# Kernel tuning notes

Hardware: AMD Instinct MI355X
Metric: run time of the kernel (lower is better)

## Reference

```python
import jax, jax.numpy as jnp
import numpy as np

B, DF, H, W = 32, 8, 144, 144
OFF = 2
K = 2 * OFF + 1            # window width 5
DS, DT, NC = 512, 1024, 6
HEADS, DH, MLP = 16, 64, 2048
THR = 0.3
CIN = DF * W               # 1152, Conv1d in-channels
ITC = DF * H * K           # 5760, token feature size
EPS = 1e-5


def _heads(X, w1, b1, g, bt, mu, vr, w2, b2):
    # X: (B, CIN, H). Per-class 1x1 conv -> BatchNorm(eval stats) -> 1x1 conv -> softmax over last dim.
    h = jnp.einsum('bch,ksc->bksh', X, w1) + b1[None, :, :, None]
    h = (h - mu[None, :, :, None]) * (g / jnp.sqrt(vr + EPS))[None, :, :, None] + bt[None, :, :, None]
    lg = jnp.einsum('bksh,kos->bkoh', h, w2) + b2[None, :, :, None]
    return jax.nn.softmax(jnp.swapaxes(lg, 2, 3), axis=-1)   # (B, NC, H, O)


def _ln(z, g, b):
    m = z.mean(-1, keepdims=True)
    v = ((z - m) ** 2).mean(-1, keepdims=True)
    return (z - m) / jnp.sqrt(v + EPS) * g + b


def _forward(x, ext_w1, ext_b1, ext_g, ext_bt, ext_mu, ext_vr, ext_w2, ext_b2, cls_w1, cls_b1, cls_g, cls_bt, cls_mu, cls_vr, cls_w2, cls_b2, ext2_w1, ext2_b1, ext2_g, ext2_bt, ext2_mu, ext2_vr, ext2_w2, ext2_b2, cls2_w1, cls2_b1, cls2_g, cls2_bt, cls2_mu, cls2_vr, cls2_w2, cls2_b2, emb, tok_w, tok_b, ln1_g, ln1_b, qkv_w, out_w, out_b, ln2_g, ln2_b, ff_w1, ff_b1, ff_w2, ff_b2, lnf_g, lnf_b, dec_w, dec_b):
    X = x.transpose(0, 1, 3, 2).reshape(B, CIN, H)          # 'b c h w -> b (c w) h'
    ext = _heads(X, ext_w1, ext_b1, ext_g, ext_bt, ext_mu, ext_vr, ext_w2, ext_b2)   # (B,NC,H,2)
    cls = _heads(X, cls_w1, cls_b1, cls_g, cls_bt, cls_mu, cls_vr, cls_w2, cls_b2)   # (B,NC,H,W)

    exist = jnp.mean(ext[..., 0], axis=2) > THR             # (B,NC) lane-existence threshold
    corr = jnp.argmax(cls, axis=-1)                         # (B,NC,H) per-row column index

    TRASH = W + 2 * OFF                                     # start of discard region for masked writes
    pad = jnp.pad(x, ((0, 0), (0, 0), (0, 0), (OFF, OFF + K)))  # left/right zero pad + K trash cols
    cols = corr[..., None] + jnp.arange(K)                  # (B,NC,H,K) window cols in padded coords
    win = jnp.take_along_axis(pad[:, None], jnp.broadcast_to(cols[:, :, None], (B, NC, DF, H, K)), axis=4)  # (B,NC,DF,H,K)

    tok = win.reshape(B, NC, ITC) @ tok_w.T + tok_b + emb[None]   # (B,NC,DT)

    # transformer depth 1; non-existing lane tokens are masked out as keys (exact match to
    # running attention over only the existing tokens, since there is no positional encoding)
    y = _ln(tok, ln1_g, ln1_b)
    qkv = y @ qkv_w.T
    q, k, v = jnp.split(qkv, 3, axis=-1)
    q = q.reshape(B, NC, HEADS, DH).transpose(0, 2, 1, 3)
    k = k.reshape(B, NC, HEADS, DH).transpose(0, 2, 1, 3)
    v = v.reshape(B, NC, HEADS, DH).transpose(0, 2, 1, 3)
    s = jnp.einsum('bhnd,bhmd->bhnm', q, k) * (DH ** -0.5)
    s = jnp.where(exist[:, None, None, :], s, -1e9)
    a = jax.nn.softmax(s, axis=-1)
    o = jnp.einsum('bhnm,bhmd->bhnd', a, v).transpose(0, 2, 1, 3).reshape(B, NC, HEADS * DH)
    tok = tok + o @ out_w.T + out_b
    y = _ln(tok, ln2_g, ln2_b)
    tok = tok + jax.nn.gelu(y @ ff_w1.T + ff_b1, approximate=False) @ ff_w2.T + ff_b2
    dec = (_ln(tok, lnf_g, lnf_b) @ dec_w.T + dec_b).reshape(B, NC, DF, H, K)

    # sequential per-class windowed write-back; rows limited to H-1 to reproduce the
    # original's `for idx_h in range(idx_h)` loop bound; masked lanes write to trash cols
    hmask = jnp.arange(H) < (H - 1)
    bi = jnp.arange(B)[:, None, None]
    hi = jnp.arange(H)[None, :, None]
    for c in range(NC):
        m = exist[:, c, None] & hmask[None, :]                          # (B,H)
        cc = jnp.where(m[:, :, None], cols[:, c], TRASH + jnp.arange(K))
        pad = pad.at[bi, :, hi, cc].set(dec[:, c].transpose(0, 2, 3, 1))  # vals (B,H,K,DF)
    x2 = pad[:, :, :, OFF:OFF + W]

    X2 = x2.transpose(0, 1, 3, 2).reshape(B, CIN, H)
    ext2 = _heads(X2, ext2_w1, ext2_b1, ext2_g, ext2_bt, ext2_mu, ext2_vr, ext2_w2, ext2_b2)
    cls2 = _heads(X2, cls2_w1, cls2_b1, cls2_g, cls2_bt, cls2_mu, cls2_vr, cls2_w2, cls2_b2)
    return ext, cls, ext2, cls2


def setup_inputs():
    ks = iter(jax.random.split(jax.random.key(0), 64))
    def w(*s):
        return jax.random.normal(next(ks), s, dtype=jnp.float32) * 0.02
    d = {"x": jax.random.normal(next(ks), (B, DF, H, W), dtype=jnp.float32)}
    for p in ["ext", "cls", "ext2", "cls2"]:
        O = 2 if p.startswith("ext") else W
        d[p + "_w1"] = w(NC, DS, CIN); d[p + "_b1"] = jnp.zeros((NC, DS))
        d[p + "_g"] = jnp.ones((NC, DS)); d[p + "_bt"] = jnp.zeros((NC, DS))
        d[p + "_mu"] = jnp.zeros((NC, DS)); d[p + "_vr"] = jnp.ones((NC, DS))
        d[p + "_w2"] = w(NC, O, DS); d[p + "_b2"] = jnp.zeros((NC, O))
    INNER = HEADS * DH
    d["emb"] = w(NC, DT); d["tok_w"] = w(DT, ITC); d["tok_b"] = jnp.zeros((DT,))
    d["ln1_g"] = jnp.ones((DT,)); d["ln1_b"] = jnp.zeros((DT,))
    d["qkv_w"] = w(3 * INNER, DT); d["out_w"] = w(DT, INNER); d["out_b"] = jnp.zeros((DT,))
    d["ln2_g"] = jnp.ones((DT,)); d["ln2_b"] = jnp.zeros((DT,))
    d["ff_w1"] = w(MLP, DT); d["ff_b1"] = jnp.zeros((MLP,))
    d["ff_w2"] = w(DT, MLP); d["ff_b2"] = jnp.zeros((DT,))
    d["lnf_g"] = jnp.ones((DT,)); d["lnf_b"] = jnp.zeros((DT,))
    d["dec_w"] = w(ITC, DT); d["dec_b"] = jnp.zeros((ITC,))
    return d


def reference(x, ext_w1, ext_b1, ext_g, ext_bt, ext_mu, ext_vr, ext_w2, ext_b2, cls_w1, cls_b1, cls_g, cls_bt, cls_mu, cls_vr, cls_w2, cls_b2, ext2_w1, ext2_b1, ext2_g, ext2_bt, ext2_mu, ext2_vr, ext2_w2, ext2_b2, cls2_w1, cls2_b1, cls2_g, cls2_bt, cls2_mu, cls2_vr, cls2_w2, cls2_b2, emb, tok_w, tok_b, ln1_g, ln1_b, qkv_w, out_w, out_b, ln2_g, ln2_b, ff_w1, ff_b1, ff_w2, ff_b2, lnf_g, lnf_b, dec_w, dec_b):
    return _forward(x, ext_w1, ext_b1, ext_g, ext_bt, ext_mu, ext_vr, ext_w2, ext_b2, cls_w1, cls_b1, cls_g, cls_bt, cls_mu, cls_vr, cls_w2, cls_b2, ext2_w1, ext2_b1, ext2_g, ext2_bt, ext2_mu, ext2_vr, ext2_w2, ext2_b2, cls2_w1, cls2_b1, cls2_g, cls2_bt, cls2_mu, cls2_vr, cls2_w2, cls2_b2, emb, tok_w, tok_b, ln1_g, ln1_b, qkv_w, out_w, out_b, ln2_g, ln2_b, ff_w1, ff_b1, ff_w2, ff_b2, lnf_g, lnf_b, dec_w, dec_b)
```

## Files before the change

kernel.cpp:

```cpp
#include <hip/hip_runtime.h>
#include <math.h>

#define Bb 32
#define DFc 8
#define Hh 144
#define Ww 144
#define OFFc 2
#define KWc 5
#define DSc 512
#define DTc 1024
#define NCc 6
#define HEADSc 16
#define DHc 64
#define MLPc 2048
#define CINc (DFc * Ww)
#define ITCc (DFc * Hh * KWc)
#define BHc (Bb * Hh)
#define INNERc (HEADSc * DHc)
#define EPSc 1e-5f
#define THRc 0.3f
#define WLNc 4608
#define GAPDELTA 1e-3f

typedef __attribute__((ext_vector_type(8))) short short8;
typedef __attribute__((ext_vector_type(4))) float f32x4;

#define ATOMIC_ADD_F32(p, v) unsafeAtomicAdd((p), (v))

__device__ inline unsigned short f2bf(float v) {
    unsigned int u = __float_as_uint(v);
    unsigned int r = (u + 0x7FFFu + ((u >> 16) & 1u)) >> 16;
    return (unsigned short)r;
}
__device__ inline float bf2f(unsigned short b) {
    return __uint_as_float(((unsigned int)b) << 16);
}

__global__ void k_split_x(const float* __restrict__ x, unsigned short* __restrict__ p,
                          long planeStride)
{
    int tid = blockIdx.x * 256 + threadIdx.x;
    if (tid >= BHc * CINc) return;
    int n = tid / CINc, k = tid % CINc;
    int b = n / Hh, h = n % Hh;
    int f = k / Ww, w = k % Ww;
    float v = x[((long)(b * DFc + f) * Hh + h) * Ww + w];
    unsigned short h0 = f2bf(v);
    p[tid] = h0;
    p[planeStride + tid] = f2bf(v - bf2f(h0));
}

__global__ __launch_bounds__(256) void k_transpose(
    const float* __restrict__ src, float* __restrict__ dst)
{
    __shared__ float t[32][33];
    const int nc = blockIdx.z;
    const int s0 = blockIdx.y * 32;
    const int k0 = blockIdx.x * 32;
    const int lx = threadIdx.x & 31, ly = threadIdx.x >> 5;
    const float* sp = src + ((long)nc * 512 + s0) * 1152 + k0;
#pragma unroll
    for (int i = 0; i < 32; i += 8)
        t[ly + i][lx] = sp[(long)(ly + i) * 1152 + lx];
    __syncthreads();
    float* dp = dst + ((long)nc * 1152 + k0) * 512 + s0;
#pragma unroll
    for (int i = 0; i < 32; i += 8)
        dp[(long)(ly + i) * 512 + lx] = t[lx][ly + i];
}

__global__ void k_w2s(const float* __restrict__ w2, const float* __restrict__ scale,
                      float* __restrict__ Ws, int O, int Mpad)
{
    int i = blockIdx.x * 256 + threadIdx.x;
    if (i >= NCc * Mpad * 512) return;
    int s = i & 511;
    int o = (i >> 9) % Mpad;
    int nc = i / (Mpad * 512);
    float v = 0.f;
    if (o < O) v = w2[((long)nc * O + o) * 512 + s] * scale[nc * 512 + s];
    Ws[i] = v;
}

__global__ __launch_bounds__(256) void gemm_nt_b(
    const float* __restrict__ A, long sAz,
    const float* __restrict__ Bm, long sBz,
    float* __restrict__ C, long sCz, int K)
{
    __shared__ float As[16][68];
    __shared__ float Bs[16][68];
    const int tid = threadIdx.x;
    const int n0 = blockIdx.x * 64;
    const int m0 = blockIdx.y * 64;
    const int z = blockIdx.z;
    const int lRow = tid >> 2, lCol = (tid & 3) << 2;
    const int ty = tid >> 4, tx = tid & 15;
    const float* Az = A + (long)z * sAz;
    const float* Bz = Bm + (long)z * sBz;

    float acc[4][4];
#pragma unroll
    for (int i = 0; i < 4; i++)
#pragma unroll
        for (int j = 0; j < 4; j++) acc[i][j] = 0.f;

    for (int k0 = 0; k0 < K; k0 += 16) {
        float4 av = *(const float4*)(Az + (long)(m0 + lRow) * K + k0 + lCol);
        As[lCol + 0][lRow] = av.x; As[lCol + 1][lRow] = av.y;
        As[lCol + 2][lRow] = av.z; As[lCol + 3][lRow] = av.w;
        float4 bv = *(const float4*)(Bz + (long)(n0 + lRow) * K + k0 + lCol);
        Bs[lCol + 0][lRow] = bv.x; Bs[lCol + 1][lRow] = bv.y;
        Bs[lCol + 2][lRow] = bv.z; Bs[lCol + 3][lRow] = bv.w;
        __syncthreads();
#pragma unroll
        for (int kk = 0; kk < 16; kk++) {
            float4 a = *(const float4*)&As[kk][ty * 4];
            float4 b = *(const float4*)&Bs[kk][tx * 4];
            float aa[4] = {a.x, a.y, a.z, a.w};
            float bb[4] = {b.x, b.y, b.z, b.w};
#pragma unroll
            for (int i = 0; i < 4; i++)
#pragma unroll
                for (int j = 0; j < 4; j++) acc[i][j] += aa[i] * bb[j];
        }
        __syncthreads();
    }
    const int ncol = n0 + tx * 4;
#pragma unroll
    for (int i = 0; i < 4; i++) {
        float* cp = C + (long)z * sCz + (long)(m0 + ty * 4 + i) * 1152 + ncol;
#pragma unroll
        for (int j = 0; j < 4; j++) cp[j] = acc[i][j];
    }
}

__global__ __launch_bounds__(256) void k_effb(
    const float* __restrict__ w2c, const float* __restrict__ b2c, const float* __restrict__ shiftC,
    const float* __restrict__ w2e, const float* __restrict__ b2e, const float* __restrict__ shiftE,
    float* __restrict__ effB)
{
    int g = blockIdx.x * 16 + (threadIdx.x >> 4);
    int lane = threadIdx.x & 15;
    if (g >= NCc * 256) return;
    int nc = g >> 8, o = g & 255;
    float d = 0.f;
    if (o < 144) {
        const float* wp = w2c + ((long)nc * 144 + o) * 512;
        const float* sp = shiftC + nc * 512;
        for (int s = lane; s < 512; s += 16) d += wp[s] * sp[s];
    } else if (o < 146) {
        const float* wp = w2e + ((long)nc * 2 + (o - 144)) * 512;
        const float* sp = shiftE + nc * 512;
        for (int s = lane; s < 512; s += 16) d += wp[s] * sp[s];
    }
#pragma unroll
    for (int off = 8; off; off >>= 1) d += __shfl_xor(d, off);
    if (lane == 0) {
        float b = (o < 144) ? b2c[nc * 144 + o] : ((o < 146) ? b2e[nc * 2 + o - 144] : 0.f);
        effB[g] = d + b;
    }
}

__global__ void k_split_effw(const float* __restrict__ effW, unsigned short* __restrict__ p,
                             long planeStride)
{
    int i = blockIdx.x * 256 + threadIdx.x;
    if (i >= NCc * 256 * 1152) return;
    int o = (i / 1152) & 255;
    float v = (o < 208) ? effW[i] : 0.f;
    unsigned short h0 = f2bf(v);
    p[i] = h0;
    p[planeStride + i] = f2bf(v - bf2f(h0));
}

__global__ __launch_bounds__(256) void gemm_fused(
    const unsigned short* __restrict__ Ag, long strideA,
    const unsigned short* __restrict__ Bg, long strideB,
    float* __restrict__ lgT, float* __restrict__ extLg,
    const float* __restrict__ effB)
{
    constexpr int K = 1152;
    constexpr int PAt[3] = {0, 0, 1};
    constexpr int PBt[3] = {0, 1, 0};
    __shared__ __align__(16) unsigned short As[2][2][128 * 32];
    __shared__ __align__(16) unsigned short Bs[2][2][128 * 32];
    const int tid = threadIdx.x;
    const int w = tid >> 6;
    const int l = tid & 63;
    const int quad = l >> 4, l15 = l & 15;
    const int z = blockIdx.z;
    const int m0 = blockIdx.y * 128, n0 = blockIdx.x * 128;
    const int rw = (w >> 1) * 64, cw = (w & 1) * 64;

    f32x4 acc[4][4];
#pragma unroll
    for (int i = 0; i < 4; i++)
#pragma unroll
        for (int j = 0; j < 4; j++) acc[i][j] = (f32x4){0.f, 0.f, 0.f, 0.f};

    const int srow = w * 32;
    const int lr = l >> 2;
    const int lc = ((l & 3) ^ ((lr >> 1) & 3)) * 8;
    const unsigned short* gA[2];
    const unsigned short* gB[2];
#pragma unroll
    for (int p = 0; p < 2; p++) {
        gA[p] = Ag + (long)p * strideA + ((long)(z * 256 + m0 + srow + lr)) * K + lc;
        gB[p] = Bg + (long)p * strideB + ((long)(n0 + srow + lr)) * K + lc;
    }
    const int ldsOff0 = srow * 32;
    const int ldsOff1 = (srow + 16) * 32;
    const int rdoff = (quad ^ ((l15 >> 1) & 3)) * 8;

    auto STAGE = [&](int buf, int k0) {
#pragma unroll
        for (int p = 0; p < 2; p++) {
            __builtin_amdgcn_global_load_lds(
                (const __attribute__((address_space(1))) void*)(gA[p] + k0),
                (__attribute__((address_space(3))) void*)&As[buf][p][ldsOff0], 16, 0, 0);
            __builtin_amdgcn_global_load_lds(
                (const __attribute__((address_space(1))) void*)(gA[p] + 16 * K + k0),
                (__attribute__((address_space(3))) void*)&As[buf][p][ldsOff1], 16, 0, 0);
            __builtin_amdgcn_global_load_lds(
                (const __attribute__((address_space(1))) void*)(gB[p] + k0),
                (__attribute__((address_space(3))) void*)&Bs[buf][p][ldsOff0], 16, 0, 0);
            __builtin_amdgcn_global_load_lds(
                (const __attribute__((address_space(1))) void*)(gB[p] + 16 * K + k0),
                (__attribute__((address_space(3))) void*)&Bs[buf][p][ldsOff1], 16, 0, 0);
        }
    };

    const int nk = K >> 5;
    STAGE(0, 0);
    __syncthreads();
    int cur = 0;
    for (int t = 0; t < nk; ++t) {
        if (t + 1 < nk) STAGE(cur ^ 1, (t + 1) << 5);

        short8 af[2][4], bf[2][4];
#pragma unroll
        for (int p = 0; p < 2; p++)
#pragma unroll
            for (int i = 0; i < 4; i++) {
                af[p][i] = *(const short8*)&As[cur][p][(rw + i * 16 + l15) * 32 + rdoff];
                bf[p][i] = *(const short8*)&Bs[cur][p][(cw + i * 16 + l15) * 32 + rdoff];
            }
#pragma unroll
        for (int t2 = 0; t2 < 3; t2++) {
            const int pa = PAt[t2], pb = PBt[t2];
#pragma unroll
            for (int i = 0; i < 4; i++)
#pragma unroll
                for (int j = 0; j < 4; j++)
                    acc[i][j] = __builtin_amdgcn_mfma_f32_16x16x32_bf16(
                        af[pa][i], bf[pb][j], acc[i][j], 0, 0, 0);
        }
        __syncthreads();
        cur ^= 1;
    }

#pragma unroll
    for (int i = 0; i < 4; i++) {
        int ob = m0 + rw + i * 16 + quad * 4;
        if (ob < 144) {
            float4 bb = *(const float4*)(effB + z * 256 + ob);
#pragma unroll
            for (int j = 0; j < 4; j++) {
                int col = n0 + cw + j * 16 + l15;
                float4 v = make_float4(acc[i][j][0] + bb.x, acc[i][j][1] + bb.y,
                                       acc[i][j][2] + bb.z, acc[i][j][3] + bb.w);
                *(float4*)(lgT + ((long)(z * BHc + col)) * 144 + ob) = v;
            }
        } else if (ob == 144) {
            float b0 = effB[z * 256 + 144];
            float b1 = effB[z * 256 + 145];
#pragma unroll
            for (int j = 0; j < 4; j++) {
                int col = n0 + cw + j * 16 + l15;
                float* ep = extLg + ((long)z * BHc + col) * 2;
                ep[0] = acc[i][j][0] + b0;
                ep[1] = acc[i][j][1] + b1;
            }
        }
    }
}

__global__ void k_bias(float* __restrict__ C, const float* __restrict__ bias,
                       int M, int N, int add)
{
    int idx = blockIdx.x * 256 + threadIdx.x;
    if (idx >= M * N) return;
    int n = idx % N;
    float v = bias ? bias[n] : 0.f;
    C[idx] = add ? C[idx] + v : v;
}

__global__ void k_tok_init(float* __restrict__ tok, const float* __restrict__ tok_b,
                           const float* __restrict__ emb)
{
    int tid = blockIdx.x * 256 + threadIdx.x;
    if (tid >= Bb * NCc * DTc) return;
    int row = tid >> 10, n = tid & 1023;
    tok[tid] = tok_b[n] + emb[(row % NCc) * DTc + n];
}

__global__ __launch_bounds__(256) void gemm_nt_sk(
    const float* __restrict__ A, const float* __restrict__ Bm, float* __restrict__ C,
    int M, int N, int K, int kc)
{
    __shared__ float As[16][68];
    __shared__ float Bs[16][68];
    const int tid = threadIdx.x;
    const int n0 = blockIdx.x * 64;
    const int m0 = blockIdx.y * 64;
    const int ks = blockIdx.z * kc;
    const int ke = min(K, ks + kc);
    const int lRow = tid >> 2, lCol = (tid & 3) << 2;
    const int ty = tid >> 4, tx = tid & 15;

    float acc[4][4];
#pragma unroll
    for (int i = 0; i < 4; i++)
#pragma unroll
        for (int j = 0; j < 4; j++) acc[i][j] = 0.f;

    for (int k0 = ks; k0 < ke; k0 += 16) {
        float4 av = *(const float4*)(A + (long)(m0 + lRow) * K + k0 + lCol);
        As[lCol + 0][lRow] = av.x; As[lCol + 1][lRow] = av.y;
        As[lCol + 2][lRow] = av.z; As[lCol + 3][lRow] = av.w;
        float4 bv = *(const float4*)(Bm + (long)(n0 + lRow) * K + k0 + lCol);
        Bs[lCol + 0][lRow] = bv.x; Bs[lCol + 1][lRow] = bv.y;
        Bs[lCol + 2][lRow] = bv.z; Bs[lCol + 3][lRow] = bv.w;
        __syncthreads();
#pragma unroll
        for (int kk = 0; kk < 16; kk++) {
            float4 a = *(const float4*)&As[kk][ty * 4];
            float4 b = *(const float4*)&Bs[kk][tx * 4];
            float aa[4] = {a.x, a.y, a.z, a.w};
            float bb[4] = {b.x, b.y, b.z, b.w};
#pragma unroll
            for (int i = 0; i < 4; i++)
#pragma unroll
                for (int j = 0; j < 4; j++) acc[i][j] += aa[i] * bb[j];
        }
        __syncthreads();
    }
    const int ncol = n0 + tx * 4;
#pragma unroll
    for (int i = 0; i < 4; i++) {
        int row = m0 + ty * 4 + i;
        float* cp = C + (long)row * N + ncol;
#pragma unroll
        for (int j = 0; j < 4; j++) ATOMIC_ADD_F32(cp + j, acc[i][j]);
    }
}

__global__ void k_scale_shift(const float* __restrict__ g, const float* __restrict__ vr,
                              const float* __restrict__ mu, const float* __restrict__ bt,
                              const float* __restrict__ b1,
                              float* __restrict__ scale, float* __restrict__ shift, int n,
                              int* __restrict__ wlc)
{
    int i = blockIdx.x * 256 + threadIdx.x;
    if (wlc && i < 8) wlc[i] = 0;
    if (i >= n) return;
    float sc = g[i] * rsqrtf(vr[i] + EPSc);
    scale[i] = sc;
    shift[i] = (b1[i] - mu[i]) * sc + bt[i];
}

__global__ __launch_bounds__(256) void k_ext_head2(
    const float* __restrict__ extLg, float* __restrict__ outExt, int* __restrict__ exist)
{
    __shared__ float red[256];
    const int bc = blockIdx.x;
    const int b = bc / NCc, nc = bc % NCc;
    const int h = threadIdx.x;
    float p0 = 0.f;
    if (h < Hh) {
        const int col = b * Hh + h;
        const float* ep = extLg + ((long)nc * BHc + col) * 2;
        float lg0 = ep[0], lg1 = ep[1];
        float mx = fmaxf(lg0, lg1);
        float e0 = expf(lg0 - mx), e1 = expf(lg1 - mx);
        float inv = 1.f / (e0 + e1);
        p0 = e0 * inv;
        float* op = outExt + ((long)bc * Hh + h) * 2;
        op[0] = p0;
        op[1] = e1 * inv;
    }
    red[threadIdx.x] = p0;
    __syncthreads();
    for (int st = 128; st > 0; st >>= 1) {
        if (threadIdx.x < st) red[threadIdx.x] += red[threadIdx.x + st];
        __syncthreads();
    }
    if (threadIdx.x == 0) exist[bc] = (red[0] / Hh > THRc) ? 1 : 0;
}

__global__ __launch_bounds__(256) void k_softmax2(
    const float* __restrict__ lgT, float* __restrict__ outCls, int* __restrict__ corr,
    int* __restrict__ wlc, int* __restrict__ wl, int stage1)
{
    int wg = blockIdx.x * 4 + (threadIdx.x >> 6);
    int l = threadIdx.x & 63;
    int nc = wg / BHc, col = wg % BHc;
    int b = col / Hh, h = col % Hh;
    const float* p = lgT + ((long)nc * BHc + col) * 144;
    float v0 = p[l];
    float v1 = p[l + 64];
    float v2 = (l < 16) ? p[l + 128] : -1e30f;
    float m1 = v0, m2; int i1 = l;
    if (v1 > m1) { m2 = m1; m1 = v1; i1 = l + 64; } else m2 = v1;
    if (v2 > m1) { m2 = m1; m1 = v2; i1 = l + 128; } else m2 = fmaxf(m2, v2);
#pragma unroll
    for (int off = 32; off; off >>= 1) {
        float o1 = __shfl_xor(m1, off);
        float o2 = __shfl_xor(m2, off);
        int oi = __shfl_xor(i1, off);
        if (o1 > m1 || (o1 == m1 && oi < i1)) { m2 = fmaxf(m1, o2); m1 = o1; i1 = oi; }
        else m2 = fmaxf(m2, o1);
    }
    float e0 = expf(v0 - m1);
    float e1 = expf(v1 - m1);
    float e2 = (l < 16) ? expf(v2 - m1) : 0.f;
    float s = e0 + e1 + e2;
#pragma unroll
    for (int off = 32; off; off >>= 1) s += __shfl_xor(s, off);
    float inv = 1.f / s;
    int row = (b * NCc + nc) * Hh + h;
    float* op = outCls + (long)row * 144;
    op[l] = e0 * inv;
    op[l + 64] = e1 * inv;
    if (l < 16) op[l + 128] = e2 * inv;
    if (l == 0) {
        corr[row] = i1;
        if (stage1 && (m1 - m2) < GAPDELTA) {
            int ix = atomicAdd(&wlc[nc], 1);
            if (ix < WLNc) wl[nc * WLNc + ix] = col;
        }
    }
}

__global__ __launch_bounds__(256) void k_fixup_h(
    const float* __restrict__ x, const float* __restrict__ w1,
    const float* __restrict__ scale, const float* __restrict__ shift,
    const int* __restrict__ wlc, const int* __restrict__ wl,
    float* __restrict__ hsfix)
{
    const int nc = blockIdx.y;
    const int cnt = min(wlc[nc], WLNc);
    const int chunk = blockIdx.z;
    if (chunk >= cnt) return;
    const int t = threadIdx.x;
    const int r = t >> 4;
    const int lane16 = t & 15;
    const int s = blockIdx.x * 16 + r;
    const float* wp = w1 + ((long)(nc * 512 + s)) * CINc + lane16 * 4;
    float4 wr[18];
#pragma unroll
    for (int i = 0; i < 18; i++) wr[i] = *(const float4*)(wp + 64 * i);
    const float sc = scale[nc * 512 + s];
    const float sh = shift[nc * 512 + s];
    int xoff[18];
#pragma unroll
    for (int i = 0; i < 18; i++) {
        int k = lane16 * 4 + 64 * i;
        xoff[i] = (k / Ww) * (Hh * Ww) + (k % Ww);
    }
    for (int it = chunk; it < cnt; it += 8) {
        int col = wl[nc * WLNc + it];
        int b = col / Hh, h = col % Hh;
        const float* xb = x + (long)b * (DFc * Hh * Ww) + h * Ww;
        float d = 0.f;
#pragma unroll
        for (int i = 0; i < 18; i++) {
            float4 xv = *(const float4*)(xb + xoff[i]);
            d += wr[i].x * xv.x + wr[i].y * xv.y + wr[i].z * xv.z + wr[i].w * xv.w;
        }
#pragma unroll
        for (int off = 8; off; off >>= 1) d += __shfl_xor(d, off);
        if (lane16 == 0) hsfix[((long)nc * WLNc + it) * 512 + s] = d * sc + sh;
    }
}

__global__ __launch_bounds__(256) void k_fixup_lg(
    const float* __restrict__ hsfix, const float* __restrict__ w2,
    const float* __restrict__ b2,
    const int* __restrict__ wlc, const int* __restrict__ wl,
    float* __restrict__ lgfix)
{
    const int nc = blockIdx.y;
    const int cnt = min(wlc[nc], WLNc);
    const int chunk = blockIdx.z;
    if (chunk >= cnt) return;
    const int t = threadIdx.x;
    const int r = t >> 4;
    const int lane16 = t & 15;
    const int o = blockIdx.x * 16 + r;
    const float* wp = w2 + ((long)(nc * 144 + o)) * 512 + lane16 * 4;
    float4 wr[8];
#pragma unroll
    for (int i = 0; i < 8; i++) wr[i] = *(const float4*)(wp + 64 * i);
    const float bb = b2[nc * 144 + o];
    for (int it = chunk; it < cnt; it += 8) {
        const float* hp = hsfix + ((long)nc * WLNc + it) * 512 + lane16 * 4;
        float d = 0.f;
#pragma unroll
        for (int i = 0; i < 8; i++) {
            float4 hv = *(const float4*)(hp + 64 * i);
            d += wr[i].x * hv.x + wr[i].y * hv.y + wr[i].z * hv.z + wr[i].w * hv.w;
        }
#pragma unroll
        for (int off = 8; off; off >>= 1) d += __shfl_xor(d, off);
        if (lane16 == 0) lgfix[((long)nc * WLNc + it) * 144 + o] = d + bb;
    }
}

__global__ __launch_bounds__(256) void k_fixup_fin(
    const float* __restrict__ lgfix,
    const int* __restrict__ wlc, const int* __restrict__ wl,
    float* __restrict__ outCls, int* __restrict__ corr)
{
    int c[6];
    int total = 0;
#pragma unroll
    for (int i = 0; i < 6; i++) { c[i] = min(wlc[i], WLNc); total += c[i]; }
    const int wid = threadIdx.x >> 6;
    const int l = threadIdx.x & 63;
    for (int g = blockIdx.x * 4 + wid; g < total; g += gridDim.x * 4) {
        int nc = 0, base = 0;
        while (nc < 5 && g >= base + c[nc]) { base += c[nc]; nc++; }
        int it = g - base;
        int col = wl[nc * WLNc + it];
        int b = col / Hh, h = col % Hh;
        const float* p = lgfix + ((long)nc * WLNc + it) * 144;
        float v0 = p[l];
        float v1 = p[l + 64];
        float v2 = (l < 16) ? p[l + 128] : -1e30f;
        float m1 = v0; int i1 = l;
        if (v1 > m1) { m1 = v1; i1 = l + 64; }
        if (v2 > m1) { m1 = v2; i1 = l + 128; }
#pragma unroll
        for (int off = 32; off; off >>= 1) {
            float o1 = __shfl_xor(m1, off);
            int oi = __shfl_xor(i1, off);
            if (o1 > m1 || (o1 == m1 && oi < i1)) { m1 = o1; i1 = oi; }
        }
        float e0 = expf(v0 - m1);
        float e1 = expf(v1 - m1);
        float e2 = (l < 16) ? expf(v2 - m1) : 0.f;
        float s = e0 + e1 + e2;
#pragma unroll
        for (int off = 32; off; off >>= 1) s += __shfl_xor(s, off);
        float inv = 1.f / s;
        int row = (b * NCc + nc) * Hh + h;
        float* op = outCls + (long)row * 144;
        op[l] = e0 * inv;
        op[l + 64] = e1 * inv;
        if (l < 16) op[l + 128] = e2 * inv;
        if (l == 0) corr[row] = i1;
    }
}

__global__ void k_gather(const float* __restrict__ x, const int* __restrict__ corr,
                         float* __restrict__ win)
{
    int tid = blockIdx.x * 256 + threadIdx.x;
    if (tid >= Bb * NCc * ITCc) return;
    int row = tid / ITCc, i = tid % ITCc;
    int b = row / NCc, nc = row % NCc;
    int f = i / (Hh * KWc);
    int r = i % (Hh * KWc);
    int h = r / KWc, k = r % KWc;
    int j = corr[(b * NCc + nc) * Hh + h] + k - OFFc;
    float v = 0.f;
    if (j >= 0 && j < Ww) v = x[((long)(b * DFc + f) * Hh + h) * Ww + j];
    win[tid] = v;
}

__global__ __launch_bounds__(256) void k_layernorm(
    const float* __restrict__ in, const float* __restrict__ g,
    const float* __restrict__ bta, float* __restrict__ out)
{
    __shared__ float r1[256], r2[256];
    const int row = blockIdx.x;
    const int t = threadIdx.x;
    const float* p = in + (long)row * DTc;
    float s = 0.f, sq = 0.f;
    for (int i = t; i < DTc; i += 256) {
        float v = p[i];
        s += v; sq += v * v;
    }
    r1[t] = s; r2[t] = sq;
    __syncthreads();
    for (int st = 128; st > 0; st >>= 1) {
        if (t < st) { r1[t] += r1[t + st]; r2[t] += r2[t + st]; }
        __syncthreads();
    }
    float mean = r1[0] / DTc;
    float var = r2[0] / DTc - mean * mean;
    float rstd = rsqrtf(var + EPSc);
    float* o = out + (long)row * DTc;
    for (int i = t; i < DTc; i += 256) o[i] = (p[i] - mean) * rstd * g[i] + bta[i];
}

__global__ void k_attention(const float* __restrict__ qkv, const int* __restrict__ exist,
                            float* __restrict__ obuf)
{
    int idx = blockIdx.x * 256 + threadIdx.x;
    if (idx >= Bb * HEADSc * NCc) return;
    int b = idx / (HEADSc * NCc);
    int r = idx % (HEADSc * NCc);
    int hd = r / NCc, n = r % NCc;
    const float* base = qkv + (long)b * NCc * (3 * INNERc);
    const float* q = base + (long)n * (3 * INNERc) + hd * DHc;
    float s[NCc];
    for (int m = 0; m < NCc; m++) {
        const float* kp = base + (long)m * (3 * INNERc) + INNERc + hd * DHc;
        float d = 0.f;
        for (int t = 0; t < DHc; t++) d += q[t] * kp[t];
        s[m] = exist[b * NCc + m] ? d * 0.125f : -1e9f;
    }
    float mx = s[0];
    for (int m = 1; m < NCc; m++) mx = fmaxf(mx, s[m]);
    float sum = 0.f;
    for (int m = 0; m < NCc; m++) { s[m] = expf(s[m] - mx); sum += s[m]; }
    float inv = 1.f / sum;
    for (int m = 0; m < NCc; m++) s[m] *= inv;
    float* op = obuf + (long)(b * NCc + n) * INNERc + hd * DHc;
    for (int t = 0; t < DHc; t++) {
        float acc = 0.f;
        for (int m = 0; m < NCc; m++)
            acc += s[m] * base[(long)m * (3 * INNERc) + 2 * INNERc + hd * DHc + t];
        op[t] = acc;
    }
}

__global__ void k_gelu(float* __restrict__ p, int n)
{
    int tid = blockIdx.x * 256 + threadIdx.x;
    if (tid < n) {
        float v = p[tid];
        p[tid] = 0.5f * v * (1.f + erff(v * 0.70710678118654752440f));
    }
}

__global__ void k_copy4(const float4* __restrict__ s, float4* __restrict__ d, int n)
{
    int tid = blockIdx.x * 256 + threadIdx.x;
    if (tid < n) d[tid] = s[tid];
}

__global__ void k_scatter(const float* __restrict__ dec, const int* __restrict__ corr,
                          const int* __restrict__ exist, float* __restrict__ x2)
{
    int idx = blockIdx.x * 256 + threadIdx.x;
    if (idx >= Bb * Hh * DFc) return;
    int b = idx / (Hh * DFc);
    int r = idx % (Hh * DFc);
    int h = r / DFc, f = r % DFc;
    if (h >= Hh - 1) return;
    unsigned long long m0 = 0ull, m1 = 0ull, m2 = 0ull;
    float* xrow = x2 + ((long)(b * DFc + f) * Hh + h) * Ww;
    for (int c = NCc - 1; c >= 0; c--) {
        if (!exist[b * NCc + c]) continue;
        int cr = corr[(b * NCc + c) * Hh + h];
        const float* dp = dec + (long)(b * NCc + c) * ITCc + f * (Hh * KWc) + h * KWc;
        for (int k = 0; k < KWc; k++) {
            int j = cr + k - OFFc;
            if (j < 0 || j >= Ww) continue;
            bool seen;
            if (j < 64) { unsigned long long bit = 1ull << j; seen = (m0 & bit) != 0; m0 |= bit; }
            else if (j < 128) { unsigned long long bit = 1ull << (j - 64); seen = (m1 & bit) != 0; m1 |= bit; }
            else { unsigned long long bit = 1ull << (j - 128); seen = (m2 & bit) != 0; m2 |= bit; }
            if (!seen) xrow[j] = dp[k];
        }
    }
}

extern "C" void kernel_launch(void* const* d_in, const int* in_sizes, int n_in,
                              void* d_out, int out_size, void* d_ws, size_t ws_size,
                              hipStream_t stream)
{
    const float* const* in = (const float* const*)d_in;
    const float* x = in[0];
    const float* emb = in[33];
    const float* tok_w = in[34]; const float* tok_b = in[35];
    const float* ln1_g = in[36]; const float* ln1_b = in[37];
    const float* qkv_w = in[38];
    const float* out_w = in[39]; const float* out_b = in[40];
    const float* ln2_g = in[41]; const float* ln2_b = in[42];
    const float* ff_w1 = in[43]; const float* ff_b1 = in[44];
    const float* ff_w2 = in[45]; const float* ff_b2 = in[46];
    const float* lnf_g = in[47]; const float* lnf_b = in[48];
    const float* dec_w = in[49]; const float* dec_b = in[50];

    float* out = (float*)d_out;
    float* outExt1 = out;
    float* outCls1 = out + 55296;
    float* outExt2 = out + 4036608;
    float* outCls2 = out + 4091904;

    const long strideB  = (long)BHc * CINc;
    const long strideApl = (long)NCc * 256 * 1152;
    float* ws = (float*)d_ws;
    float* w1Tc  = ws;
    float* w1Te  = ws + 3538944;
    float* effWf = ws + 7077888;
    float* lgTn  = ws + 8847360;
    float* hsfix = ws;
    float* x2    = ws;
    unsigned short* Apl = (unsigned short*)(ws + 14155776);
    float* W2s    = ws + 17694720;
    float* extLg  = ws + 17694720;
    float* scaleE = ws + 17694720 + 589824;
    float* shiftE = scaleE + 3072;
    float* effB   = shiftE + 3072;
    unsigned short* Bpl = (unsigned short*)(ws + 18481152);
    float* lgfix = ws + 18481152;
    float* windec = ws + 18481152;
    float* tok  = windec + 1105920;
    float* ybuf = tok + 196608;
    float* qkvB = ybuf + 196608;
    float* obuf = qkvB + 589824;
    float* ffh  = obuf + 196608;
    float* scaleB = ws + 26443776;
    float* shiftB = scaleB + 3072;
    int* corrB  = (int*)(shiftB + 3072);
    int* existB = corrB + 27648;
    int* wlcB   = existB + 192;
    int* wlB    = wlcB + 8;
    float* win = windec;
    float* dec = windec;

    auto run_stage = [&](int be, int bc, float* oExt, float* oCls, bool stage1) {
        k_scale_shift<<<12, 256, 0, stream>>>(in[bc + 2], in[bc + 5], in[bc + 4],
                                              in[bc + 3], in[bc + 1], scaleB, shiftB,
                                              NCc * DSc, wlcB);
        k_scale_shift<<<12, 256, 0, stream>>>(in[be + 2], in[be + 5], in[be + 4],
                                              in[be + 3], in[be + 1], scaleE, shiftE,
                                              NCc * DSc, nullptr);
        k_transpose<<<dim3(36, 16, 6), 256, 0, stream>>>(in[bc + 0], w1Tc);
        k_transpose<<<dim3(36, 16, 6), 256, 0, stream>>>(in[be + 0], w1Te);
        k_w2s<<<2304, 256, 0, stream>>>(in[bc + 6], scaleB, W2s, 144, 192);
        gemm_nt_b<<<dim3(18, 3, 6), 256, 0, stream>>>(W2s, (long)192 * 512, w1Tc,
                                                      (long)1152 * 512, effWf,
                                                      (long)256 * 1152, 512);
        k_w2s<<<768, 256, 0, stream>>>(in[be + 6], scaleE, W2s, 2, 64);
        gemm_nt_b<<<dim3(18, 1, 6), 256, 0, stream>>>(W2s, (long)64 * 512, w1Te,
                                                      (long)1152 * 512,
                                                      effWf + (long)144 * 1152,
                                                      (long)256 * 1152, 512);
        k_effb<<<96, 256, 0, stream>>>(in[bc + 6], in[bc + 7], shiftB,
                                       in[be + 6], in[be + 7], shiftE, effB);
        k_split_effw<<<6912, 256, 0, stream>>>(effWf, Apl, strideApl);
        gemm_fused<<<dim3(36, 2, 6), 256, 0, stream>>>(Apl, strideApl, Bpl, strideB,
                                                       lgTn, extLg, effB);
        k_ext_head2<<<Bb * NCc, 256, 0, stream>>>(extLg, oExt, existB);
        k_softmax2<<<6912, 256, 0, stream>>>(lgTn, oCls, corrB, wlcB, wlB, stage1 ? 1 : 0);
        if (stage1) {
            k_fixup_h<<<dim3(32, NCc, 8), 256, 0, stream>>>(x, in[bc + 0], scaleB, shiftB,
                                                            wlcB, wlB, hsfix);
            k_fixup_lg<<<dim3(9, NCc, 8), 256, 0, stream>>>(hsfix, in[bc + 6], in[bc + 7],
                                                            wlcB, wlB, lgfix);
            k_fixup_fin<<<512, 256, 0, stream>>>(lgfix, wlcB, wlB, oCls, corrB);
        }
    };

    k_split_x<<<20736, 256, 0, stream>>>(x, Bpl, strideB);
    run_stage(1, 9, outExt1, outCls1, true);

    k_gather<<<4320, 256, 0, stream>>>(x, corrB, win);
    k_tok_init<<<768, 256, 0, stream>>>(tok, tok_b, emb);
    gemm_nt_sk<<<dim3(16, 3, 8), 256, 0, stream>>>(win, tok_w, tok, 192, DTc, ITCc, 720);

    k_layernorm<<<192, 256, 0, stream>>>(tok, ln1_g, ln1_b, ybuf);
    k_bias<<<2304, 256, 0, stream>>>(qkvB, nullptr, 192, 3 * INNERc, 0);
    gemm_nt_sk<<<dim3(48, 3, 4), 256, 0, stream>>>(ybuf, qkv_w, qkvB, 192, 3 * INNERc, DTc, 256);
    k_attention<<<12, 256, 0, stream>>>(qkvB, existB, obuf);
    k_bias<<<768, 256, 0, stream>>>(tok, out_b, 192, DTc, 1);
    gemm_nt_sk<<<dim3(16, 3, 8), 256, 0, stream>>>(obuf, out_w, tok, 192, DTc, INNERc, 128);
    k_layernorm<<<192, 256, 0, stream>>>(tok, ln2_g, ln2_b, ybuf);
    k_bias<<<1536, 256, 0, stream>>>(ffh, ff_b1, 192, MLPc, 0);
    gemm_nt_sk<<<dim3(32, 3, 4), 256, 0, stream>>>(ybuf, ff_w1, ffh, 192, MLPc, DTc, 256);
    k_gelu<<<1536, 256, 0, stream>>>(ffh, 192 * MLPc);
    k_bias<<<768, 256, 0, stream>>>(tok, ff_b2, 192, DTc, 1);
    gemm_nt_sk<<<dim3(16, 3, 8), 256, 0, stream>>>(ffh, ff_w2, tok, 192, DTc, MLPc, 256);
    k_layernorm<<<192, 256, 0, stream>>>(tok, lnf_g, lnf_b, ybuf);
    k_bias<<<4320, 256, 0, stream>>>(dec, dec_b, 192, ITCc, 0);
    gemm_nt_sk<<<dim3(90, 3, 2), 256, 0, stream>>>(ybuf, dec_w, dec, 192, ITCc, DTc, 512);

    k_copy4<<<5184, 256, 0, stream>>>((const float4*)x, (float4*)x2, 1327104);
    k_scatter<<<144, 256, 0, stream>>>(dec, corrB, existB, x2);

    k_split_x<<<20736, 256, 0, stream>>>(x2, Bpl, strideB);
    run_stage(17, 25, outExt2, outCls2, false);

    (void)in_sizes; (void)n_in; (void)out_size; (void)ws_size;
}
```

Measured before the change: 1.019 ms.

## Prefetch next K-tile in GEMMs, raise split-K counts, fuse decoder bias

```diff
diff --git a/kernel.cpp b/kernel.cpp
--- a/kernel.cpp
+++ b/kernel.cpp
@@ -95,8 +95,8 @@
     const int z = blockIdx.z;
     const int lRow = tid >> 2, lCol = (tid & 3) << 2;
     const int ty = tid >> 4, tx = tid & 15;
-    const float* Az = A + (long)z * sAz;
-    const float* Bz = Bm + (long)z * sBz;
+    const float* Az = A + (long)z * sAz + (long)(m0 + lRow) * K + lCol;
+    const float* Bz = Bm + (long)z * sBz + (long)(n0 + lRow) * K + lCol;
 
     float acc[4][4];
 #pragma unroll
@@ -104,14 +104,18 @@
 #pragma unroll
         for (int j = 0; j < 4; j++) acc[i][j] = 0.f;
 
+    float4 av = *(const float4*)(Az);
+    float4 bv = *(const float4*)(Bz);
     for (int k0 = 0; k0 < K; k0 += 16) {
-        float4 av = *(const float4*)(Az + (long)(m0 + lRow) * K + k0 + lCol);
         As[lCol + 0][lRow] = av.x; As[lCol + 1][lRow] = av.y;
         As[lCol + 2][lRow] = av.z; As[lCol + 3][lRow] = av.w;
-        float4 bv = *(const float4*)(Bz + (long)(n0 + lRow) * K + k0 + lCol);
         Bs[lCol + 0][lRow] = bv.x; Bs[lCol + 1][lRow] = bv.y;
         Bs[lCol + 2][lRow] = bv.z; Bs[lCol + 3][lRow] = bv.w;
         __syncthreads();
+        if (k0 + 16 < K) {
+            av = *(const float4*)(Az + k0 + 16);
+            bv = *(const float4*)(Bz + k0 + 16);
+        }
 #pragma unroll
         for (int kk = 0; kk < 16; kk++) {
             float4 a = *(const float4*)&As[kk][ty * 4];
@@ -317,6 +321,8 @@
     const int ke = min(K, ks + kc);
     const int lRow = tid >> 2, lCol = (tid & 3) << 2;
     const int ty = tid >> 4, tx = tid & 15;
+    const float* Ap = A + (long)(m0 + lRow) * K + lCol;
+    const float* Bp = Bm + (long)(n0 + lRow) * K + lCol;
 
     float acc[4][4];
 #pragma unroll
@@ -324,14 +330,18 @@
 #pragma unroll
         for (int j = 0; j < 4; j++) acc[i][j] = 0.f;
 
+    float4 av = *(const float4*)(Ap + ks);
+    float4 bv = *(const float4*)(Bp + ks);
     for (int k0 = ks; k0 < ke; k0 += 16) {
-        float4 av = *(const float4*)(A + (long)(m0 + lRow) * K + k0 + lCol);
         As[lCol + 0][lRow] = av.x; As[lCol + 1][lRow] = av.y;
         As[lCol + 2][lRow] = av.z; As[lCol + 3][lRow] = av.w;
-        float4 bv = *(const float4*)(Bm + (long)(n0 + lRow) * K + k0 + lCol);
         Bs[lCol + 0][lRow] = bv.x; Bs[lCol + 1][lRow] = bv.y;
         Bs[lCol + 2][lRow] = bv.z; Bs[lCol + 3][lRow] = bv.w;
         __syncthreads();
+        if (k0 + 16 < ke) {
+            av = *(const float4*)(Ap + k0 + 16);
+            bv = *(const float4*)(Bp + k0 + 16);
+        }
 #pragma unroll
         for (int kk = 0; kk < 16; kk++) {
             float4 a = *(const float4*)&As[kk][ty * 4];
@@ -352,6 +362,64 @@
         float* cp = C + (long)row * N + ncol;
 #pragma unroll
         for (int j = 0; j < 4; j++) ATOMIC_ADD_F32(cp + j, acc[i][j]);
+    }
+}
+
+__global__ __launch_bounds__(256) void gemm_nt_f(
+    const float* __restrict__ A, const float* __restrict__ Bm, float* __restrict__ C,
+    const float* __restrict__ bias, int M, int N, int K)
+{
+    __shared__ float As[16][68];
+    __shared__ float Bs[16][68];
+    const int tid = threadIdx.x;
+    const int n0 = blockIdx.x * 64;
+    const int m0 = blockIdx.y * 64;
+    const int lRow = tid >> 2, lCol = (tid & 3) << 2;
+    const int ty = tid >> 4, tx = tid & 15;
+    const float* Ap = A + (long)(m0 + lRow) * K + lCol;
+    const float* Bp = Bm + (long)(n0 + lRow) * K + lCol;
+
+    float acc[4][4];
+#pragma unroll
+    for (int i = 0; i < 4; i++)
+#pragma unroll
+        for (int j = 0; j < 4; j++) acc[i][j] = 0.f;
+
+    float4 av = *(const float4*)(Ap);
+    float4 bv = *(const float4*)(Bp);
+    for (int k0 = 0; k0 < K; k0 += 16) {
+        As[lCol + 0][lRow] = av.x; As[lCol + 1][lRow] = av.y;
+        As[lCol + 2][lRow] = av.z; As[lCol + 3][lRow] = av.w;
+        Bs[lCol + 0][lRow] = bv.x; Bs[lCol + 1][lRow] = bv.y;
+        Bs[lCol + 2][lRow] = bv.z; Bs[lCol + 3][lRow] = bv.w;
+        __syncthreads();
+        if (k0 + 16 < K) {
+            av = *(const float4*)(Ap + k0 + 16);
+            bv = *(const float4*)(Bp + k0 + 16);
+        }
+#pragma unroll
+        for (int kk = 0; kk < 16; kk++) {
+            float4 a = *(const float4*)&As[kk][ty * 4];
+            float4 b = *(const float4*)&Bs[kk][tx * 4];
+            float aa[4] = {a.x, a.y, a.z, a.w};
+            float bb[4] = {b.x, b.y, b.z, b.w};
+#pragma unroll
+            for (int i = 0; i < 4; i++)
+#pragma unroll
+                for (int j = 0; j < 4; j++) acc[i][j] += aa[i] * bb[j];
+        }
+        __syncthreads();
+    }
+    const int ncol = n0 + tx * 4;
+    float4 bb4 = *(const float4*)(bias + ncol);
+#pragma unroll
+    for (int i = 0; i < 4; i++) {
+        int row = m0 + ty * 4 + i;
+        float* cp = C + (long)row * N + ncol;
+        cp[0] = acc[i][0] + bb4.x;
+        cp[1] = acc[i][1] + bb4.y;
+        cp[2] = acc[i][2] + bb4.z;
+        cp[3] = acc[i][3] + bb4.w;
     }
 }
 
@@ -773,23 +841,22 @@
 
     k_gather<<<4320, 256, 0, stream>>>(x, corrB, win);
     k_tok_init<<<768, 256, 0, stream>>>(tok, tok_b, emb);
-    gemm_nt_sk<<<dim3(16, 3, 8), 256, 0, stream>>>(win, tok_w, tok, 192, DTc, ITCc, 720);
+    gemm_nt_sk<<<dim3(16, 3, 20), 256, 0, stream>>>(win, tok_w, tok, 192, DTc, ITCc, 288);
 
     k_layernorm<<<192, 256, 0, stream>>>(tok, ln1_g, ln1_b, ybuf);
     k_bias<<<2304, 256, 0, stream>>>(qkvB, nullptr, 192, 3 * INNERc, 0);
-    gemm_nt_sk<<<dim3(48, 3, 4), 256, 0, stream>>>(ybuf, qkv_w, qkvB, 192, 3 * INNERc, DTc, 256);
+    gemm_nt_sk<<<dim3(48, 3, 8), 256, 0, stream>>>(ybuf, qkv_w, qkvB, 192, 3 * INNERc, DTc, 128);
     k_attention<<<12, 256, 0, stream>>>(qkvB, existB, obuf);
     k_bias<<<768, 256, 0, stream>>>(tok, out_b, 192, DTc, 1);
     gemm_nt_sk<<<dim3(16, 3, 8), 256, 0, stream>>>(obuf, out_w, tok, 192, DTc, INNERc, 128);
     k_layernorm<<<192, 256, 0, stream>>>(tok, ln2_g, ln2_b, ybuf);
     k_bias<<<1536, 256, 0, stream>>>(ffh, ff_b1, 192, MLPc, 0);
-    gemm_nt_sk<<<dim3(32, 3, 4), 256, 0, stream>>>(ybuf, ff_w1, ffh, 192, MLPc, DTc, 256);
+    gemm_nt_sk<<<dim3(32, 3, 8), 256, 0, stream>>>(ybuf, ff_w1, ffh, 192, MLPc, DTc, 128);
     k_gelu<<<1536, 256, 0, stream>>>(ffh, 192 * MLPc);
     k_bias<<<768, 256, 0, stream>>>(tok, ff_b2, 192, DTc, 1);
-    gemm_nt_sk<<<dim3(16, 3, 8), 256, 0, stream>>>(ffh, ff_w2, tok, 192, DTc, MLPc, 256);
+    gemm_nt_sk<<<dim3(16, 3, 16), 256, 0, stream>>>(ffh, ff_w2, tok, 192, DTc, MLPc, 128);
     k_layernorm<<<192, 256, 0, stream>>>(tok, lnf_g, lnf_b, ybuf);
-    k_bias<<<4320, 256, 0, stream>>>(dec, dec_b, 192, ITCc, 0);
-    gemm_nt_sk<<<dim3(90, 3, 2), 256, 0, stream>>>(ybuf, dec_w, dec, 192, ITCc, DTc, 512);
+    gemm_nt_f<<<dim3(90, 3), 256, 0, stream>>>(ybuf, dec_w, dec, dec_b, 192, ITCc, DTc);
 
     k_copy4<<<5184, 256, 0, stream>>>((const float4*)x, (float4*)x2, 1327104);
     k_scatter<<<144, 256, 0, stream>>>(dec, corrB, existB, x2);
```

Result: slower. 1.072 ms (+5.1%).
